# Kernel tuning notes

Measured on AMD Instinct MI355X. Metric: run time of the kernel, lower is better.

The kernel has to match this reference:

```python
import jax, jax.numpy as jnp
import numpy as np

E, EDIM, NDIM, H = 262144, 256, 256, 8
DH = NDIM // H
EPS = 1e-5  # torch nn.LayerNorm default


def _param(k, shape, scale=0.02):
    return jax.random.normal(k, shape, jnp.float32) * scale


def setup_inputs() -> dict:
    key = jax.random.key(0)
    ks = jax.random.split(key, 12)
    return {
        "x": jax.random.normal(ks[0], (E, EDIM), jnp.float32),
        "src_x": jax.random.normal(ks[1], (E, NDIM), jnp.float32),
        "dst_x": jax.random.normal(ks[2], (E, NDIM), jnp.float32),
        # multi-head cross-attention params (q from edge feats, k/v from node feats)
        "Wq": _param(ks[3], (EDIM, NDIM)), "bq": jnp.zeros((NDIM,), jnp.float32),
        "Wk": _param(ks[4], (NDIM, NDIM)), "bk": jnp.zeros((NDIM,), jnp.float32),
        "Wv": _param(ks[5], (NDIM, NDIM)), "bv": jnp.zeros((NDIM,), jnp.float32),
        "Wo": _param(ks[6], (NDIM, EDIM)), "bo": jnp.zeros((EDIM,), jnp.float32),
        "W1": _param(ks[7], (EDIM, 4 * EDIM)), "b1": jnp.zeros((4 * EDIM,), jnp.float32),
        "W2": _param(ks[8], (4 * EDIM, EDIM)), "b2": jnp.zeros((EDIM,), jnp.float32),
        # two LayerNorms
        "g1": jnp.ones((EDIM,), jnp.float32), "be1": jnp.zeros((EDIM,), jnp.float32),
        "g2": jnp.ones((EDIM,), jnp.float32), "be2": jnp.zeros((EDIM,), jnp.float32),
    }


def _layer_norm(h, g, b):
    m = jnp.mean(h, axis=-1, keepdims=True)
    v = jnp.mean(jnp.square(h - m), axis=-1, keepdims=True)
    return (h - m) * jax.lax.rsqrt(v + EPS) * g + b


def reference(x, src_x, dst_x, Wq, bq, Wk, bk, Wv, bv, Wo, bo,
              W1, b1, W2, b2, g1, be1, g2, be2):
    # per-edge cross-attention: query = edge feat (len 1), keys/values = (src, dst) (len 2)
    q = (x @ Wq + bq).reshape(E, H, DH)                 # [E,H,DH]
    kv = jnp.stack([src_x, dst_x], axis=1)              # [E,2,NDIM]
    k = (kv @ Wk + bk).reshape(E, 2, H, DH)
    v = (kv @ Wv + bv).reshape(E, 2, H, DH)
    scale = 1.0 / float(np.sqrt(DH))
    scores = jnp.einsum('ehd,ekhd->ehk', q, k) * scale  # [E,H,2]
    attn = jax.nn.softmax(scores, axis=-1)
    ctx = jnp.einsum('ehk,ekhd->ehd', attn, v).reshape(E, NDIM)
    out = ctx @ Wo + bo                                  # [E,EDIM]
    h = _layer_norm(x + out, g1, be1)
    ff = jax.nn.relu(h @ W1 + b1) @ W2 + b2
    return _layer_norm(h + ff, g2, be2)
```

## Files before the change

kernel.cpp:

```cpp
#include <hip/hip_runtime.h>
#include <hip/hip_bf16.h>
#include <math.h>

#define NROWS   262144
#define BM      64
#define THREADS 512
#define LDSB    65536

using bf16x8 = __attribute__((ext_vector_type(8))) short;
using s16x4  = __attribute__((ext_vector_type(4))) short;
using f32x4  = __attribute__((ext_vector_type(4))) float;

__device__ __forceinline__ short f2bf(float f) {
  __hip_bfloat16 h = __float2bfloat16(f);
  return __builtin_bit_cast(short, h);
}
__device__ __forceinline__ float bf2f(short s) {
  __hip_bfloat16 h = __builtin_bit_cast(__hip_bfloat16, s);
  return __bfloat162float(h);
}
__device__ __forceinline__ int swz(int row, int col) {
  return row * 512 + ((col * 2) ^ ((row & 7) << 4));
}

__device__ __forceinline__ float red16(float p) {
  p += __shfl_xor(p, 1, 64);
  p += __shfl_xor(p, 2, 64);
  p += __shfl_xor(p, 4, 64);
  p += __shfl_xor(p, 8, 64);
  return p;
}

__device__ __forceinline__ void zero_acc(f32x4 (&acc)[4][2]) {
#pragma unroll
  for (int m = 0; m < 4; ++m)
#pragma unroll
    for (int n = 0; n < 2; ++n)
      acc[m][n] = (f32x4){0.f, 0.f, 0.f, 0.f};
}

__device__ __forceinline__ void stage_tile(char* __restrict__ buf,
                                           const float* __restrict__ g, int tid) {
#pragma unroll
  for (int it = 0; it < 8; ++it) {
    int idx = it * THREADS + tid;
    int r = idx >> 6;
    int c = (idx & 63) << 2;
    float4 v = *(const float4*)(g + r * 256 + c);
    s16x4 o;
    o[0] = f2bf(v.x); o[1] = f2bf(v.y); o[2] = f2bf(v.z); o[3] = f2bf(v.w);
    *(s16x4*)(buf + swz(r, c)) = o;
  }
}

__device__ __forceinline__ void gemm256(const char* __restrict__ Abuf,
                                        const short* __restrict__ WT, int Kw,
                                        int cb, int koff, int li, int hi,
                                        f32x4 (&acc)[4][2]) {
  const short* w0 = WT + (size_t)(cb + li) * Kw + koff + hi * 8;
  const short* w1 = WT + (size_t)(cb + 16 + li) * Kw + koff + hi * 8;
#pragma unroll 4
  for (int kk = 0; kk < 256; kk += 32) {
    int ka = kk + hi * 8;
    bf16x8 b0 = *(const bf16x8*)(w0 + kk);
    bf16x8 b1 = *(const bf16x8*)(w1 + kk);
    bf16x8 a[4];
#pragma unroll
    for (int m = 0; m < 4; ++m)
      a[m] = *(const bf16x8*)(Abuf + swz(16 * m + li, ka));
#pragma unroll
    for (int m = 0; m < 4; ++m) {
      acc[m][0] = __builtin_amdgcn_mfma_f32_16x16x32_bf16(a[m], b0, acc[m][0], 0, 0, 0);
      acc[m][1] = __builtin_amdgcn_mfma_f32_16x16x32_bf16(a[m], b1, acc[m][1], 0, 0, 0);
    }
  }
}

__global__ void prep(const float* __restrict__ Wq, const float* __restrict__ Wk,
                     const float* __restrict__ Wv, const float* __restrict__ Wo,
                     const float* __restrict__ W1, const float* __restrict__ W2,
                     short* __restrict__ wt) {
  int idx = blockIdx.x * blockDim.x + threadIdx.x;
  if (idx < 262144) {
    int m = idx >> 16;
    const float* W = (m == 0) ? Wq : (m == 1) ? Wk : (m == 2) ? Wv : Wo;
    int l = idx & 65535;
    int n = l >> 8, k = l & 255;
    wt[idx] = f2bf(W[k * 256 + n]);
  } else if (idx < 524288) {
    int l = idx - 262144;
    int n = l >> 8, k = l & 255;
    wt[idx] = f2bf(W1[k * 1024 + n]);
  } else {
    int l = idx - 524288;
    int n = l >> 10, k = l & 1023;
    wt[idx] = f2bf(W2[k * 256 + n]);
  }
}

__global__ __launch_bounds__(THREADS, 4)
void fused(const float* __restrict__ x, const float* __restrict__ sx,
           const float* __restrict__ dx,
           const float* __restrict__ bq, const float* __restrict__ bk,
           const float* __restrict__ bv, const float* __restrict__ bo,
           const float* __restrict__ b1, const float* __restrict__ b2,
           const float* __restrict__ g1, const float* __restrict__ be1,
           const float* __restrict__ g2, const float* __restrict__ be2,
           const short* __restrict__ wt, float* __restrict__ out) {
  extern __shared__ char sm[];
  char* Cbuf = sm;
  char* Tbuf = sm + 32768;
  float* scr  = (float*)(sm + 32768);
  float* scr2 = (float*)(sm + 32768 + 4096);

  const short* WqT = wt;
  const short* WkT = wt + 65536;
  const short* WvT = wt + 131072;
  const short* WoT = wt + 196608;
  const short* W1T = wt + 262144;
  const short* W2T = wt + 524288;

  const int tid  = threadIdx.x;
  const int w    = tid >> 6;
  const int lane = tid & 63;
  const int li   = lane & 15;
  const int hi   = lane >> 4;
  const int cb   = w * 32;
  const size_t row0 = (size_t)blockIdx.x * BM;

  const float* xt = x  + row0 * 256;
  const float* st = sx + row0 * 256;
  const float* dt = dx + row0 * 256;

  stage_tile(Tbuf, xt, tid);
  __syncthreads();

  f32x4 qa[4][2], ka[4][2], va[4][2];
  zero_acc(qa);
  gemm256(Tbuf, WqT, 256, cb, 0, li, hi, qa);
  {
    float bq0 = bq[cb + li], bq1 = bq[cb + 16 + li];
#pragma unroll
    for (int m = 0; m < 4; ++m)
#pragma unroll
      for (int j = 0; j < 4; ++j) { qa[m][0][j] += bq0; qa[m][1][j] += bq1; }
  }
  __syncthreads();

  stage_tile(Tbuf, st, tid);
  __syncthreads();

  zero_acc(ka);
  gemm256(Tbuf, WkT, 256, cb, 0, li, hi, ka);
  float ss[4][4];
  {
    float bk0 = bk[cb + li], bk1 = bk[cb + 16 + li];
#pragma unroll
    for (int m = 0; m < 4; ++m)
#pragma unroll
      for (int j = 0; j < 4; ++j) {
        float p = qa[m][0][j] * (ka[m][0][j] + bk0) + qa[m][1][j] * (ka[m][1][j] + bk1);
        ss[m][j] = red16(p) * 0.17677669529663687f;
      }
  }
  zero_acc(va);
  gemm256(Tbuf, WvT, 256, cb, 0, li, hi, va);
#pragma unroll
  for (int m = 0; m < 4; ++m)
#pragma unroll
    for (int n = 0; n < 2; ++n)
#pragma unroll
      for (int j = 0; j < 4; ++j)
        *(short*)(Cbuf + swz(16 * m + 4 * hi + j, cb + 16 * n + li)) = f2bf(va[m][n][j]);
  __syncthreads();

  stage_tile(Tbuf, dt, tid);
  __syncthreads();

  zero_acc(ka);
  gemm256(Tbuf, WkT, 256, cb, 0, li, hi, ka);
  float aw[4][4];
  {
    float bk0 = bk[cb + li], bk1 = bk[cb + 16 + li];
#pragma unroll
    for (int m = 0; m < 4; ++m)
#pragma unroll
      for (int j = 0; j < 4; ++j) {
        float p = qa[m][0][j] * (ka[m][0][j] + bk0) + qa[m][1][j] * (ka[m][1][j] + bk1);
        float sd = red16(p) * 0.17677669529663687f;
        aw[m][j] = 1.f / (1.f + expf(sd - ss[m][j]));
      }
  }
  zero_acc(va);
  gemm256(Tbuf, WvT, 256, cb, 0, li, hi, va);
  {
    float bv0 = bv[cb + li], bv1 = bv[cb + 16 + li];
#pragma unroll
    for (int m = 0; m < 4; ++m)
#pragma unroll
      for (int j = 0; j < 4; ++j) {
        int r = 16 * m + 4 * hi + j;
        float a = aw[m][j];
#pragma unroll
        for (int n = 0; n < 2; ++n) {
          short* p = (short*)(Cbuf + swz(r, cb + 16 * n + li));
          float vs = bf2f(*p);
          float ctx = a * vs + (1.f - a) * va[m][n][j] + (n ? bv1 : bv0);
          *p = f2bf(ctx);
        }
      }
  }
  __syncthreads();

  f32x4 oa[4][2];
  zero_acc(oa);
  gemm256(Cbuf, WoT, 256, cb, 0, li, hi, oa);
  {
    float bo0 = bo[cb + li], bo1 = bo[cb + 16 + li];
#pragma unroll
    for (int m = 0; m < 4; ++m)
#pragma unroll
      for (int j = 0; j < 4; ++j) {
        int r = 16 * m + 4 * hi + j;
        float v0 = oa[m][0][j] + bo0 + xt[r * 256 + cb + li];
        float v1 = oa[m][1][j] + bo1 + xt[r * 256 + cb + 16 + li];
        oa[m][0][j] = v0; oa[m][1][j] = v1;
        float s = red16(v0 + v1);
        float q = red16(v0 * v0 + v1 * v1);
        if (li == 0) { scr[(w * 64 + r) * 2] = s; scr[(w * 64 + r) * 2 + 1] = q; }
      }
  }
  __syncthreads();
  if (tid < BM) {
    float S = 0.f, Q = 0.f;
#pragma unroll
    for (int ww = 0; ww < 8; ++ww) {
      S += scr[(ww * 64 + tid) * 2];
      Q += scr[(ww * 64 + tid) * 2 + 1];
    }
    float mean = S * (1.f / 256.f);
    float var  = Q * (1.f / 256.f) - mean * mean;
    scr2[tid * 2] = mean;
    scr2[tid * 2 + 1] = rsqrtf(var + 1e-5f);
  }
  __syncthreads();
  {
    float g10 = g1[cb + li], g11 = g1[cb + 16 + li];
    float a10 = be1[cb + li], a11 = be1[cb + 16 + li];
#pragma unroll
    for (int m = 0; m < 4; ++m)
#pragma unroll
      for (int j = 0; j < 4; ++j) {
        int r = 16 * m + 4 * hi + j;
        float mean = scr2[r * 2], rs = scr2[r * 2 + 1];
        *(short*)(Cbuf + swz(r, cb + li))      = f2bf((oa[m][0][j] - mean) * rs * g10 + a10);
        *(short*)(Cbuf + swz(r, cb + 16 + li)) = f2bf((oa[m][1][j] - mean) * rs * g11 + a11);
      }
  }
  __syncthreads();

  f32x4 a2[4][2];
  zero_acc(a2);
#pragma unroll 1
  for (int c = 0; c < 4; ++c) {
    f32x4 a1[4][2];
    zero_acc(a1);
    gemm256(Cbuf, W1T, 256, 256 * c + cb, 0, li, hi, a1);
    {
      float b10 = b1[256 * c + cb + li], b11 = b1[256 * c + cb + 16 + li];
#pragma unroll
      for (int m = 0; m < 4; ++m)
#pragma unroll
        for (int j = 0; j < 4; ++j) {
          int r = 16 * m + 4 * hi + j;
          *(short*)(Tbuf + swz(r, cb + li))      = f2bf(fmaxf(a1[m][0][j] + b10, 0.f));
          *(short*)(Tbuf + swz(r, cb + 16 + li)) = f2bf(fmaxf(a1[m][1][j] + b11, 0.f));
        }
    }
    __syncthreads();
    gemm256(Tbuf, W2T, 1024, cb, 256 * c, li, hi, a2);
    __syncthreads();
  }

  {
    float b20 = b2[cb + li], b21 = b2[cb + 16 + li];
#pragma unroll
    for (int m = 0; m < 4; ++m)
#pragma unroll
      for (int j = 0; j < 4; ++j) {
        int r = 16 * m + 4 * hi + j;
        float h0 = bf2f(*(short*)(Cbuf + swz(r, cb + li)));
        float h1 = bf2f(*(short*)(Cbuf + swz(r, cb + 16 + li)));
        float v0 = a2[m][0][j] + b20 + h0;
        float v1 = a2[m][1][j] + b21 + h1;
        a2[m][0][j] = v0; a2[m][1][j] = v1;
        float s = red16(v0 + v1);
        float q = red16(v0 * v0 + v1 * v1);
        if (li == 0) { scr[(w * 64 + r) * 2] = s; scr[(w * 64 + r) * 2 + 1] = q; }
      }
  }
  __syncthreads();
  if (tid < BM) {
    float S = 0.f, Q = 0.f;
#pragma unroll
    for (int ww = 0; ww < 8; ++ww) {
      S += scr[(ww * 64 + tid) * 2];
      Q += scr[(ww * 64 + tid) * 2 + 1];
    }
    float mean = S * (1.f / 256.f);
    float var  = Q * (1.f / 256.f) - mean * mean;
    scr2[tid * 2] = mean;
    scr2[tid * 2 + 1] = rsqrtf(var + 1e-5f);
  }
  __syncthreads();

  {
    float g20 = g2[cb + li], g21 = g2[cb + 16 + li];
    float a20 = be2[cb + li], a21 = be2[cb + 16 + li];
    float* orow = out + row0 * 256;
#pragma unroll 1
    for (int hf = 0; hf < 2; ++hf) {
#pragma unroll
      for (int m2 = 0; m2 < 2; ++m2) {
        int m = 2 * hf + m2;
#pragma unroll
        for (int j = 0; j < 4; ++j) {
          int r = 16 * m + 4 * hi + j;
          float mean = scr2[r * 2], rs = scr2[r * 2 + 1];
          int rr = r - 32 * hf;
          float v0 = (a2[m][0][j] - mean) * rs * g20 + a20;
          float v1 = (a2[m][1][j] - mean) * rs * g21 + a21;
          *(float*)(Cbuf + rr * 1024 + (((cb + li) * 4) ^ ((rr & 7) << 4)))      = v0;
          *(float*)(Cbuf + rr * 1024 + (((cb + 16 + li) * 4) ^ ((rr & 7) << 4))) = v1;
        }
      }
      __syncthreads();
#pragma unroll
      for (int t = 0; t < 4; ++t) {
        int idx = t * THREADS + tid;
        int r = idx >> 6, c4 = idx & 63;
        f32x4 v = *(f32x4*)(Cbuf + r * 1024 + ((c4 * 16) ^ ((r & 7) << 4)));
        *(f32x4*)(orow + (hf * 32 + r) * 256 + c4 * 4) = v;
      }
      __syncthreads();
    }
  }
}

extern "C" void kernel_launch(void* const* d_in, const int* in_sizes, int n_in,
                              void* d_out, int out_size, void* d_ws, size_t ws_size,
                              hipStream_t stream) {
  const float* x   = (const float*)d_in[0];
  const float* sx  = (const float*)d_in[1];
  const float* dx  = (const float*)d_in[2];
  const float* Wq  = (const float*)d_in[3];
  const float* bq  = (const float*)d_in[4];
  const float* Wk  = (const float*)d_in[5];
  const float* bk  = (const float*)d_in[6];
  const float* Wv  = (const float*)d_in[7];
  const float* bv  = (const float*)d_in[8];
  const float* Wo  = (const float*)d_in[9];
  const float* bo  = (const float*)d_in[10];
  const float* W1  = (const float*)d_in[11];
  const float* b1  = (const float*)d_in[12];
  const float* W2  = (const float*)d_in[13];
  const float* b2  = (const float*)d_in[14];
  const float* g1  = (const float*)d_in[15];
  const float* be1 = (const float*)d_in[16];
  const float* g2  = (const float*)d_in[17];
  const float* be2 = (const float*)d_in[18];
  short* wt = (short*)d_ws;

  prep<<<dim3(1536), dim3(512), 0, stream>>>(Wq, Wk, Wv, Wo, W1, W2, wt);
  fused<<<dim3(NROWS / BM), dim3(THREADS), LDSB, stream>>>(
      x, sx, dx, bq, bk, bv, bo, b1, b2, g1, be1, g2, be2, wt, (float*)d_out);
}
```

Before: 1.325 ms.

## Double-buffer src/dst tiles, keep values in registers, drop key bias

Reorders the attention stage so the dst tile is staged into the second LDS buffer while the Q GEMM runs, and the src tile is staged while the dst K GEMM runs. This overlaps global loads with MFMA work and removes some barriers. The key bias is dropped because it cancels in the two-key softmax. The src and dst value projections now stay in fp32 registers instead of round-tripping through bf16 LDS. Unroll factors are lowered and occupancy is set via waves_per_eu, which trades instruction-level parallelism for register headroom; keeping more live accumulators risks spills.

```diff
diff --git a/kernel.cpp b/kernel.cpp
--- a/kernel.cpp
+++ b/kernel.cpp
@@ -41,7 +41,7 @@
 
 __device__ __forceinline__ void stage_tile(char* __restrict__ buf,
                                            const float* __restrict__ g, int tid) {
-#pragma unroll
+#pragma unroll 2
   for (int it = 0; it < 8; ++it) {
     int idx = it * THREADS + tid;
     int r = idx >> 6;
@@ -59,7 +59,7 @@
                                         f32x4 (&acc)[4][2]) {
   const short* w0 = WT + (size_t)(cb + li) * Kw + koff + hi * 8;
   const short* w1 = WT + (size_t)(cb + 16 + li) * Kw + koff + hi * 8;
-#pragma unroll 4
+#pragma unroll 2
   for (int kk = 0; kk < 256; kk += 32) {
     int ka = kk + hi * 8;
     bf16x8 b0 = *(const bf16x8*)(w0 + kk);
@@ -98,20 +98,22 @@
   }
 }
 
-__global__ __launch_bounds__(THREADS, 4)
+__global__ __attribute__((amdgpu_waves_per_eu(4, 4))) __launch_bounds__(THREADS)
 void fused(const float* __restrict__ x, const float* __restrict__ sx,
            const float* __restrict__ dx,
-           const float* __restrict__ bq, const float* __restrict__ bk,
+           const float* __restrict__ bq,
            const float* __restrict__ bv, const float* __restrict__ bo,
            const float* __restrict__ b1, const float* __restrict__ b2,
            const float* __restrict__ g1, const float* __restrict__ be1,
            const float* __restrict__ g2, const float* __restrict__ be2,
            const short* __restrict__ wt, float* __restrict__ out) {
   extern __shared__ char sm[];
-  char* Cbuf = sm;
-  char* Tbuf = sm + 32768;
-  float* scr  = (float*)(sm + 32768);
-  float* scr2 = (float*)(sm + 32768 + 4096);
+  char* Tbuf = sm;
+  char* Cbuf = sm + 32768;
+  float* scrT  = (float*)Tbuf;
+  float* scr2T = (float*)(Tbuf + 4096);
+  float* scrC  = (float*)Cbuf;
+  float* scr2C = (float*)(Cbuf + 4096);
 
   const short* WqT = wt;
   const short* WkT = wt + 65536;
@@ -135,81 +137,76 @@
   stage_tile(Tbuf, xt, tid);
   __syncthreads();
 
-  f32x4 qa[4][2], ka[4][2], va[4][2];
+  f32x4 qa[4][2];
   zero_acc(qa);
   gemm256(Tbuf, WqT, 256, cb, 0, li, hi, qa);
-  {
+  stage_tile(Cbuf, dt, tid);
+  {
+    const float scl = 0.17677669529663687f;
     float bq0 = bq[cb + li], bq1 = bq[cb + 16 + li];
 #pragma unroll
     for (int m = 0; m < 4; ++m)
 #pragma unroll
-      for (int j = 0; j < 4; ++j) { qa[m][0][j] += bq0; qa[m][1][j] += bq1; }
-  }
-  __syncthreads();
-
-  stage_tile(Tbuf, st, tid);
-  __syncthreads();
-
-  zero_acc(ka);
-  gemm256(Tbuf, WkT, 256, cb, 0, li, hi, ka);
-  float ss[4][4];
-  {
-    float bk0 = bk[cb + li], bk1 = bk[cb + 16 + li];
-#pragma unroll
-    for (int m = 0; m < 4; ++m)
-#pragma unroll
-      for (int j = 0; j < 4; ++j) {
-        float p = qa[m][0][j] * (ka[m][0][j] + bk0) + qa[m][1][j] * (ka[m][1][j] + bk1);
-        ss[m][j] = red16(p) * 0.17677669529663687f;
-      }
-  }
-  zero_acc(va);
-  gemm256(Tbuf, WvT, 256, cb, 0, li, hi, va);
+      for (int j = 0; j < 4; ++j) {
+        qa[m][0][j] = (qa[m][0][j] + bq0) * scl;
+        qa[m][1][j] = (qa[m][1][j] + bq1) * scl;
+      }
+  }
+  __syncthreads();
+
+  float pd[4][4];
+  {
+    f32x4 ka[4][2];
+    zero_acc(ka);
+    gemm256(Cbuf, WkT, 256, cb, 0, li, hi, ka);
+    stage_tile(Tbuf, st, tid);
+#pragma unroll
+    for (int m = 0; m < 4; ++m)
+#pragma unroll
+      for (int j = 0; j < 4; ++j)
+        pd[m][j] = red16(qa[m][0][j] * ka[m][0][j] + qa[m][1][j] * ka[m][1][j]);
+  }
+  __syncthreads();
+
+  float aw[4][4];
+  {
+    f32x4 ka[4][2];
+    zero_acc(ka);
+    gemm256(Tbuf, WkT, 256, cb, 0, li, hi, ka);
+#pragma unroll
+    for (int m = 0; m < 4; ++m)
+#pragma unroll
+      for (int j = 0; j < 4; ++j) {
+        float ps = red16(qa[m][0][j] * ka[m][0][j] + qa[m][1][j] * ka[m][1][j]);
+        aw[m][j] = 1.f / (1.f + expf(pd[m][j] - ps));
+      }
+  }
+  f32x4 vs[4][2];
+  zero_acc(vs);
+  gemm256(Tbuf, WvT, 256, cb, 0, li, hi, vs);
+  {
+    f32x4 vd[4][2];
+    zero_acc(vd);
+    gemm256(Cbuf, WvT, 256, cb, 0, li, hi, vd);
+    float bv0 = bv[cb + li], bv1 = bv[cb + 16 + li];
+#pragma unroll
+    for (int m = 0; m < 4; ++m)
+#pragma unroll
+      for (int j = 0; j < 4; ++j) {
+        float a = aw[m][j];
+        vs[m][0][j] = a * vs[m][0][j] + (1.f - a) * vd[m][0][j] + bv0;
+        vs[m][1][j] = a * vs[m][1][j] + (1.f - a) * vd[m][1][j] + bv1;
+      }
+  }
+  __syncthreads();
+
 #pragma unroll
   for (int m = 0; m < 4; ++m)
 #pragma unroll
     for (int n = 0; n < 2; ++n)
 #pragma unroll
       for (int j = 0; j < 4; ++j)
-        *(short*)(Cbuf + swz(16 * m + 4 * hi + j, cb + 16 * n + li)) = f2bf(va[m][n][j]);
-  __syncthreads();
-
-  stage_tile(Tbuf, dt, tid);
-  __syncthreads();
-
-  zero_acc(ka);
-  gemm256(Tbuf, WkT, 256, cb, 0, li, hi, ka);
-  float aw[4][4];
-  {
-    float bk0 = bk[cb + li], bk1 = bk[cb + 16 + li];
-#pragma unroll
-    for (int m = 0; m < 4; ++m)
-#pragma unroll
-      for (int j = 0; j < 4; ++j) {
-        float p = qa[m][0][j] * (ka[m][0][j] + bk0) + qa[m][1][j] * (ka[m][1][j] + bk1);
-        float sd = red16(p) * 0.17677669529663687f;
-        aw[m][j] = 1.f / (1.f + expf(sd - ss[m][j]));
-      }
-  }
-  zero_acc(va);
-  gemm256(Tbuf, WvT, 256, cb, 0, li, hi, va);
-  {
-    float bv0 = bv[cb + li], bv1 = bv[cb + 16 + li];
-#pragma unroll
-    for (int m = 0; m < 4; ++m)
-#pragma unroll
-      for (int j = 0; j < 4; ++j) {
-        int r = 16 * m + 4 * hi + j;
-        float a = aw[m][j];
-#pragma unroll
-        for (int n = 0; n < 2; ++n) {
-          short* p = (short*)(Cbuf + swz(r, cb + 16 * n + li));
-          float vs = bf2f(*p);
-          float ctx = a * vs + (1.f - a) * va[m][n][j] + (n ? bv1 : bv0);
-          *p = f2bf(ctx);
-        }
-      }
-  }
+        *(short*)(Cbuf + swz(16 * m + 4 * hi + j, cb + 16 * n + li)) = f2bf(vs[m][n][j]);
   __syncthreads();
 
   f32x4 oa[4][2];
@@ -227,7 +224,7 @@
         oa[m][0][j] = v0; oa[m][1][j] = v1;
         float s = red16(v0 + v1);
         float q = red16(v0 * v0 + v1 * v1);
-        if (li == 0) { scr[(w * 64 + r) * 2] = s; scr[(w * 64 + r) * 2 + 1] = q; }
+        if (li == 0) { scrT[(w * 64 + r) * 2] = s; scrT[(w * 64 + r) * 2 + 1] = q; }
       }
   }
   __syncthreads();
@@ -235,13 +232,13 @@
     float S = 0.f, Q = 0.f;
 #pragma unroll
     for (int ww = 0; ww < 8; ++ww) {
-      S += scr[(ww * 64 + tid) * 2];
-      Q += scr[(ww * 64 + tid) * 2 + 1];
+      S += scrT[(ww * 64 + tid) * 2];
+      Q += scrT[(ww * 64 + tid) * 2 + 1];
     }
     float mean = S * (1.f / 256.f);
     float var  = Q * (1.f / 256.f) - mean * mean;
-    scr2[tid * 2] = mean;
-    scr2[tid * 2 + 1] = rsqrtf(var + 1e-5f);
+    scr2T[tid * 2] = mean;
+    scr2T[tid * 2 + 1] = rsqrtf(var + 1e-5f);
   }
   __syncthreads();
   {
@@ -252,7 +249,7 @@
 #pragma unroll
       for (int j = 0; j < 4; ++j) {
         int r = 16 * m + 4 * hi + j;
-        float mean = scr2[r * 2], rs = scr2[r * 2 + 1];
+        float mean = scr2T[r * 2], rs = scr2T[r * 2 + 1];
         *(short*)(Cbuf + swz(r, cb + li))      = f2bf((oa[m][0][j] - mean) * rs * g10 + a10);
         *(short*)(Cbuf + swz(r, cb + 16 + li)) = f2bf((oa[m][1][j] - mean) * rs * g11 + a11);
       }
@@ -289,28 +286,34 @@
 #pragma unroll
       for (int j = 0; j < 4; ++j) {
         int r = 16 * m + 4 * hi + j;
-        float h0 = bf2f(*(short*)(Cbuf + swz(r, cb + li)));
-        float h1 = bf2f(*(short*)(Cbuf + swz(r, cb + 16 + li)));
-        float v0 = a2[m][0][j] + b20 + h0;
-        float v1 = a2[m][1][j] + b21 + h1;
-        a2[m][0][j] = v0; a2[m][1][j] = v1;
-        float s = red16(v0 + v1);
-        float q = red16(v0 * v0 + v1 * v1);
-        if (li == 0) { scr[(w * 64 + r) * 2] = s; scr[(w * 64 + r) * 2 + 1] = q; }
-      }
-  }
+        a2[m][0][j] += b20 + bf2f(*(short*)(Cbuf + swz(r, cb + li)));
+        a2[m][1][j] += b21 + bf2f(*(short*)(Cbuf + swz(r, cb + 16 + li)));
+      }
+  }
+  __syncthreads();
+
+#pragma unroll
+  for (int m = 0; m < 4; ++m)
+#pragma unroll
+    for (int j = 0; j < 4; ++j) {
+      int r = 16 * m + 4 * hi + j;
+      float v0 = a2[m][0][j], v1 = a2[m][1][j];
+      float s = red16(v0 + v1);
+      float q = red16(v0 * v0 + v1 * v1);
+      if (li == 0) { scrC[(w * 64 + r) * 2] = s; scrC[(w * 64 + r) * 2 + 1] = q; }
+    }
   __syncthreads();
   if (tid < BM) {
     float S = 0.f, Q = 0.f;
 #pragma unroll
     for (int ww = 0; ww < 8; ++ww) {
-      S += scr[(ww * 64 + tid) * 2];
-      Q += scr[(ww * 64 + tid) * 2 + 1];
+      S += scrC[(ww * 64 + tid) * 2];
+      Q += scrC[(ww * 64 + tid) * 2 + 1];
     }
     float mean = S * (1.f / 256.f);
     float var  = Q * (1.f / 256.f) - mean * mean;
-    scr2[tid * 2] = mean;
-    scr2[tid * 2 + 1] = rsqrtf(var + 1e-5f);
+    scr2C[tid * 2] = mean;
+    scr2C[tid * 2 + 1] = rsqrtf(var + 1e-5f);
   }
   __syncthreads();
 
@@ -326,12 +329,12 @@
 #pragma unroll
         for (int j = 0; j < 4; ++j) {
           int r = 16 * m + 4 * hi + j;
-          float mean = scr2[r * 2], rs = scr2[r * 2 + 1];
+          float mean = scr2C[r * 2], rs = scr2C[r * 2 + 1];
           int rr = r - 32 * hf;
-          float v0 = (a2[m][0][j] - mean) * rs * g20 + a20;
-          float v1 = (a2[m][1][j] - mean) * rs * g21 + a21;
-          *(float*)(Cbuf + rr * 1024 + (((cb + li) * 4) ^ ((rr & 7) << 4)))      = v0;
-          *(float*)(Cbuf + rr * 1024 + (((cb + 16 + li) * 4) ^ ((rr & 7) << 4))) = v1;
+          *(float*)(Tbuf + rr * 1024 + (((cb + li) * 4) ^ ((rr & 7) << 4)))
+              = (a2[m][0][j] - mean) * rs * g20 + a20;
+          *(float*)(Tbuf + rr * 1024 + (((cb + 16 + li) * 4) ^ ((rr & 7) << 4)))
+              = (a2[m][1][j] - mean) * rs * g21 + a21;
         }
       }
       __syncthreads();
@@ -339,7 +342,7 @@
       for (int t = 0; t < 4; ++t) {
         int idx = t * THREADS + tid;
         int r = idx >> 6, c4 = idx & 63;
-        f32x4 v = *(f32x4*)(Cbuf + r * 1024 + ((c4 * 16) ^ ((r & 7) << 4)));
+        f32x4 v = *(f32x4*)(Tbuf + r * 1024 + ((c4 * 16) ^ ((r & 7) << 4)));
         *(f32x4*)(orow + (hf * 32 + r) * 256 + c4 * 4) = v;
       }
       __syncthreads();
@@ -356,7 +359,6 @@
   const float* Wq  = (const float*)d_in[3];
   const float* bq  = (const float*)d_in[4];
   const float* Wk  = (const float*)d_in[5];
-  const float* bk  = (const float*)d_in[6];
   const float* Wv  = (const float*)d_in[7];
   const float* bv  = (const float*)d_in[8];
   const float* Wo  = (const float*)d_in[9];
@@ -373,5 +375,5 @@
 
   prep<<<dim3(1536), dim3(512), 0, stream>>>(Wq, Wk, Wv, Wo, W1, W2, wt);
   fused<<<dim3(NROWS / BM), dim3(THREADS), LDSB, stream>>>(
-      x, sx, dx, bq, bk, bv, bo, b1, b2, g1, be1, g2, be2, wt, (float*)d_out);
-}
+      x, sx, dx, bq, bv, bo, b1, b2, g1, be1, g2, be2, wt, (float*)d_out);
+}
```

Result: faster. 1.139 ms (-14.0%).
